# Performance work log

Hardware: AMD Instinct MI355X
Metric: run time of the kernel (lower is better)

Reference implementation:

```python
import jax, jax.numpy as jnp
import numpy as np

H = 1024        # hidden_dim
NH = 8          # num_heads
HD = H // NH    # head_dim
EPS = 1e-5


def setup_inputs() -> dict:
    key = jax.random.key(0)
    ks = jax.random.split(key, 16)
    s = 0.02
    d = {
        'x': jax.random.normal(ks[0], (2, 2048, H), dtype=jnp.float32),
        'ln1_g': jnp.ones((H,), jnp.float32), 'ln1_b': jnp.zeros((H,), jnp.float32),
        'ln2_g': jnp.ones((H,), jnp.float32), 'ln2_b': jnp.zeros((H,), jnp.float32),
        'Wq': jax.random.normal(ks[1], (H, H), jnp.float32) * s,
        'bq': jnp.zeros((H,), jnp.float32),
        'Wk': jax.random.normal(ks[2], (H, H), jnp.float32) * s,
        'bk': jnp.zeros((H,), jnp.float32),
        'Wv': jax.random.normal(ks[3], (H, H), jnp.float32) * s,
        'bv': jnp.zeros((H,), jnp.float32),
        'Wo': jax.random.normal(ks[4], (H, H), jnp.float32) * s,
        'bo': jnp.zeros((H,), jnp.float32),
        'W1': jax.random.normal(ks[5], (H, 4 * H), jnp.float32) * s,
        'b1': jnp.zeros((4 * H,), jnp.float32),
        'W2': jax.random.normal(ks[6], (4 * H, H), jnp.float32) * s,
        'b2': jnp.zeros((H,), jnp.float32),
    }
    return d


def _layernorm(x, g, b):
    mu = jnp.mean(x, axis=-1, keepdims=True)
    var = jnp.mean(jnp.square(x - mu), axis=-1, keepdims=True)
    return (x - mu) * jax.lax.rsqrt(var + EPS) * g + b


def _block(x, ln1_g, ln1_b, ln2_g, ln2_b, Wq, bq, Wk, bk, Wv, bv, Wo, bo, W1, b1, W2, b2):
    B, S, _ = x.shape
    h = _layernorm(x, ln1_g, ln1_b)
    q = (h @ Wq + bq).reshape(B, S, NH, HD).transpose(0, 2, 1, 3)  # [B,NH,S,HD]
    k = (h @ Wk + bk).reshape(B, S, NH, HD).transpose(0, 2, 1, 3)
    v = (h @ Wv + bv).reshape(B, S, NH, HD).transpose(0, 2, 1, 3)
    scores = jnp.einsum('bhqd,bhkd->bhqk', q, k) / np.sqrt(HD)
    causal = jnp.tril(jnp.ones((S, S), bool))
    scores = jnp.where(causal, scores, -jnp.inf)
    attn = jax.nn.softmax(scores, axis=-1)
    y = jnp.einsum('bhqk,bhkd->bhqd', attn, v).transpose(0, 2, 1, 3).reshape(B, S, H)
    x = x + y @ Wo + bo
    h2 = _layernorm(x, ln2_g, ln2_b)
    m = jax.nn.gelu(h2 @ W1 + b1, approximate=False) @ W2 + b2
    return x + m


def reference(x, ln1_g, ln1_b, ln2_g, ln2_b, Wq, bq, Wk, bk, Wv, bv, Wo, bo, W1, b1, W2, b2):
    return _block(x, ln1_g, ln1_b, ln2_g, ln2_b, Wq, bq, Wk, bk, Wv, bv, Wo, bo, W1, b1, W2, b2)
```

## Files before the change

kernel.cpp:

```cpp
#include <hip/hip_runtime.h>
#include <hip/hip_bf16.h>
#include <math.h>

using bf16 = __hip_bfloat16;
typedef __attribute__((ext_vector_type(8))) short short8v;
typedef __attribute__((ext_vector_type(4))) float f32x4;

#define DEV __device__ __forceinline__

DEV void load_lds16(const bf16* gsrc, bf16* ldst) {
  __builtin_amdgcn_global_load_lds((const __attribute__((address_space(1))) void*)gsrc,
                                   (__attribute__((address_space(3))) void*)ldst, 16, 0, 0);
}

DEV void swz8(int& bx, int& by, int gx, int gy) {
  const int n = gx * gy, c = n >> 3;
  int lin = bx + gx * by;
  lin = (lin & 7) * c + (lin >> 3);
  bx = lin % gx; by = lin / gx;
}

DEV unsigned pack2bf(float a, float b) {
  bf16 ba = __float2bfloat16(a), bb = __float2bfloat16(b);
  return (unsigned)*(unsigned short*)&ba | ((unsigned)*(unsigned short*)&bb << 16);
}

__global__ __launch_bounds__(256) void prep_kernel(
    const float* __restrict__ Wq, const float* __restrict__ Wk, const float* __restrict__ Wv,
    const float* __restrict__ Wo, const float* __restrict__ W1, const float* __restrict__ W2,
    bf16* __restrict__ WqT, bf16* __restrict__ WkT, bf16* __restrict__ WvT,
    bf16* __restrict__ WoT, bf16* __restrict__ W1T, bf16* __restrict__ W2T,
    const float* __restrict__ x, const float* __restrict__ ln1g, const float* __restrict__ ln1b,
    bf16* __restrict__ h) {
  __shared__ float tile[64][65];
  const int b = blockIdx.x;
  if (b >= 3072) {
    const int row = b - 3072, t = threadIdx.x;
    const float4 v = ((const float4*)(x + (size_t)row * 1024))[t];
    float s = v.x + v.y + v.z + v.w;
#pragma unroll
    for (int mm = 1; mm < 64; mm <<= 1) s += __shfl_xor(s, mm);
    __shared__ float r1[4], r2[4];
    if ((t & 63) == 0) r1[t >> 6] = s;
    __syncthreads();
    const float mean = (r1[0] + r1[1] + r1[2] + r1[3]) * (1.0f / 1024.0f);
    const float d0 = v.x - mean, d1 = v.y - mean, d2 = v.z - mean, d3 = v.w - mean;
    float s2 = d0 * d0 + d1 * d1 + d2 * d2 + d3 * d3;
#pragma unroll
    for (int mm = 1; mm < 64; mm <<= 1) s2 += __shfl_xor(s2, mm);
    if ((t & 63) == 0) r2[t >> 6] = s2;
    __syncthreads();
    const float var = (r2[0] + r2[1] + r2[2] + r2[3]) * (1.0f / 1024.0f);
    const float rinv = rsqrtf(var + 1e-5f);
    const int c = t * 4;
    bf16* o = h + (size_t)row * 1024 + c;
    o[0] = __float2bfloat16(d0 * rinv * ln1g[c + 0] + ln1b[c + 0]);
    o[1] = __float2bfloat16(d1 * rinv * ln1g[c + 1] + ln1b[c + 1]);
    o[2] = __float2bfloat16(d2 * rinv * ln1g[c + 2] + ln1b[c + 2]);
    o[3] = __float2bfloat16(d3 * rinv * ln1g[c + 3] + ln1b[c + 3]);
    return;
  }
  const float* W; bf16* WT; int K, N, n0, k0;
  if (b < 1024) {
    const int which = b >> 8, t = b & 255;
    W  = (which == 0) ? Wq  : (which == 1) ? Wk  : (which == 2) ? Wv  : Wo;
    WT = (which == 0) ? WqT : (which == 1) ? WkT : (which == 2) ? WvT : WoT;
    K = 1024; N = 1024; n0 = (t & 15) * 64; k0 = (t >> 4) * 64;
  } else if (b < 2048) {
    const int t = b - 1024;
    W = W1; WT = W1T; K = 1024; N = 4096; n0 = (t & 63) * 64; k0 = (t >> 6) * 64;
  } else {
    const int t = b - 2048;
    W = W2; WT = W2T; K = 4096; N = 1024; n0 = (t & 15) * 64; k0 = (t >> 4) * 64;
  }
  const int tx = threadIdx.x & 15, ty = threadIdx.x >> 4;
#pragma unroll
  for (int p = 0; p < 4; ++p) {
    int r = p * 16 + ty;
    float4 vv = *(const float4*)&W[(size_t)(k0 + r) * N + n0 + tx * 4];
    tile[r][tx * 4 + 0] = vv.x; tile[r][tx * 4 + 1] = vv.y;
    tile[r][tx * 4 + 2] = vv.z; tile[r][tx * 4 + 3] = vv.w;
  }
  __syncthreads();
#pragma unroll
  for (int p = 0; p < 4; ++p) {
    int n = p * 16 + ty;
    bf16* dst = WT + (size_t)(n0 + n) * K + k0 + tx * 4;
#pragma unroll
    for (int j = 0; j < 4; ++j) dst[j] = __float2bfloat16(tile[tx * 4 + j][n]);
  }
}

__global__ __launch_bounds__(256) void ln_kernel(const float* __restrict__ x,
                                                 const float* __restrict__ g,
                                                 const float* __restrict__ b,
                                                 bf16* __restrict__ out) {
  const int row = blockIdx.x, t = threadIdx.x;
  const float4 v = ((const float4*)(x + (size_t)row * 1024))[t];
  float s = v.x + v.y + v.z + v.w;
#pragma unroll
  for (int mm = 1; mm < 64; mm <<= 1) s += __shfl_xor(s, mm);
  __shared__ float r1[4], r2[4];
  if ((t & 63) == 0) r1[t >> 6] = s;
  __syncthreads();
  const float mean = (r1[0] + r1[1] + r1[2] + r1[3]) * (1.0f / 1024.0f);
  const float d0 = v.x - mean, d1 = v.y - mean, d2 = v.z - mean, d3 = v.w - mean;
  float s2 = d0 * d0 + d1 * d1 + d2 * d2 + d3 * d3;
#pragma unroll
  for (int mm = 1; mm < 64; mm <<= 1) s2 += __shfl_xor(s2, mm);
  if ((t & 63) == 0) r2[t >> 6] = s2;
  __syncthreads();
  const float var = (r2[0] + r2[1] + r2[2] + r2[3]) * (1.0f / 1024.0f);
  const float rinv = rsqrtf(var + 1e-5f);
  const int c = t * 4;
  bf16* o = out + (size_t)row * 1024 + c;
  o[0] = __float2bfloat16(d0 * rinv * g[c + 0] + b[c + 0]);
  o[1] = __float2bfloat16(d1 * rinv * g[c + 1] + b[c + 1]);
  o[2] = __float2bfloat16(d2 * rinv * g[c + 2] + b[c + 2]);
  o[3] = __float2bfloat16(d3 * rinv * g[c + 3] + b[c + 3]);
}

template <int EPI>
__global__ __launch_bounds__(512, 2) void gemm256(
    const bf16* __restrict__ A, const bf16* __restrict__ BT,
    const float* __restrict__ bias0, const float* __restrict__ bias1, const float* __restrict__ bias2,
    void* __restrict__ outp, int M, int N, int K) {
  __shared__ bf16 As[4][256 * 32];
  __shared__ bf16 Bs[4][256 * 32];
  const int tid = threadIdx.x;
  const int w = tid >> 6, l = tid & 63;
  const int wm = w >> 2, wn = w & 3;
  const int c = l & 15, h4 = l >> 4;
  int bx = blockIdx.x, by = blockIdx.y;
  swz8(bx, by, gridDim.x, gridDim.y);
  const int m0 = by * 256, n0 = bx * 256;

  const float* bias;
  int zz = 0;
  if (EPI == 0) {
    zz = n0 >> 10;
    bias = ((zz == 0) ? bias0 : (zz == 1) ? bias1 : bias2) - (zz << 10);
  } else {
    bias = bias0;
  }

  const int rl = l >> 2;
  const int ch = (l & 3) * 8;
  const int nkt = K >> 5;

  f32x4 acc[8][4] = {};

  auto STAGE_A = [&](int t, int b) {
    const bf16* src = A + (size_t)(m0 + rl) * K + t * 32 + ch;
    load_lds16(src + (size_t)((w * 2 + 0) * 16) * K, &As[b][(w * 2 + 0) * 512]);
    load_lds16(src + (size_t)((w * 2 + 1) * 16) * K, &As[b][(w * 2 + 1) * 512]);
  };
  auto STAGE_B = [&](int t, int b) {
    const bf16* src = BT + (size_t)(n0 + rl) * K + t * 32 + ch;
    load_lds16(src + (size_t)((w * 2 + 0) * 16) * K, &Bs[b][(w * 2 + 0) * 512]);
    load_lds16(src + (size_t)((w * 2 + 1) * 16) * K, &Bs[b][(w * 2 + 1) * 512]);
  };

  STAGE_A(0, 0); STAGE_B(0, 0);
  STAGE_A(1, 1); STAGE_B(1, 1);
  STAGE_A(2, 2); STAGE_B(2, 2);
  asm volatile("s_waitcnt vmcnt(8)" ::: "memory");
  __builtin_amdgcn_sched_barrier(0);
  __builtin_amdgcn_s_barrier();

  for (int t = 0; t < nkt; ++t) {
    const bf16* Ab = &As[t & 3][0];
    const bf16* Bb = &Bs[t & 3][0];
    short8v a[4], b[4];
#pragma unroll
    for (int i = 0; i < 4; ++i)
      a[i] = *(const short8v*)&Ab[(wm * 128 + i * 16 + c) * 32 + h4 * 8];
#pragma unroll
    for (int i = 0; i < 4; ++i)
      b[i] = *(const short8v*)&Bb[(wn * 64 + i * 16 + c) * 32 + h4 * 8];
    if (t + 3 < nkt) STAGE_A(t + 3, (t + 3) & 3);
    asm volatile("s_waitcnt lgkmcnt(0)" ::: "memory");
    __builtin_amdgcn_sched_barrier(0);
    __builtin_amdgcn_s_setprio(1);
#pragma unroll
    for (int mi = 0; mi < 4; ++mi)
#pragma unroll
      for (int ni = 0; ni < 4; ++ni)
        acc[mi][ni] = __builtin_amdgcn_mfma_f32_16x16x32_bf16(a[mi], b[ni], acc[mi][ni], 0, 0, 0);
    __builtin_amdgcn_s_setprio(0);
#pragma unroll
    for (int i = 0; i < 4; ++i)
      a[i] = *(const short8v*)&Ab[(wm * 128 + 64 + i * 16 + c) * 32 + h4 * 8];
    if (t + 3 < nkt) STAGE_B(t + 3, (t + 3) & 3);
    asm volatile("s_waitcnt lgkmcnt(0)" ::: "memory");
    __builtin_amdgcn_sched_barrier(0);
    __builtin_amdgcn_s_setprio(1);
#pragma unroll
    for (int mi = 0; mi < 4; ++mi)
#pragma unroll
      for (int ni = 0; ni < 4; ++ni)
        acc[4 + mi][ni] = __builtin_amdgcn_mfma_f32_16x16x32_bf16(a[mi], b[ni], acc[4 + mi][ni], 0, 0, 0);
    __builtin_amdgcn_s_setprio(0);
    if (t < nkt - 3)       asm volatile("s_waitcnt vmcnt(8)" ::: "memory");
    else if (t == nkt - 3) asm volatile("s_waitcnt vmcnt(4)" ::: "memory");
    else                   asm volatile("s_waitcnt vmcnt(0)" ::: "memory");
    __builtin_amdgcn_sched_barrier(0);
    __builtin_amdgcn_s_barrier();
  }

#pragma unroll
  for (int mi = 0; mi < 8; ++mi) {
#pragma unroll
    for (int ni = 0; ni < 4; ++ni) {
#pragma unroll
      for (int r = 0; r < 4; ++r) {
        const int m = m0 + wm * 128 + mi * 16 + h4 * 4 + r;
        const int n = n0 + wn * 64 + ni * 16 + c;
        const float vv = acc[mi][ni][r] + bias[n];
        if (EPI == 0) {
          const int bb = m >> 11, ss = m & 2047;
          const int n1 = n - (zz << 10);
          const int hh = n1 >> 7, dd = n1 & 127;
          ((bf16*)outp)[(size_t)zz * 4194304 + (((size_t)bb * 8 + hh) * 2048 + ss) * 128 + dd] =
              __float2bfloat16(vv);
        } else {
          const size_t idx = (size_t)m * N + n;
          const float u = 0.7978845608028654f * (vv + 0.044715f * vv * vv * vv);
          const float tt = __expf(2.0f * u);
          const float th = 1.0f - 2.0f / (tt + 1.0f);
          ((bf16*)outp)[idx] = __float2bfloat16(0.5f * vv * (1.0f + th));
        }
      }
    }
  }
}

template <int EPI, int MI>
__global__ __launch_bounds__(256) void gemm128(
    const bf16* __restrict__ A, const bf16* __restrict__ BT,
    const float* __restrict__ bias0, const float* __restrict__ bias1, const float* __restrict__ bias2,
    const float* __restrict__ res, void* __restrict__ outp,
    int M, int N, int K) {
  __shared__ bf16 As[2][MI * 1024];
  __shared__ bf16 Bs[2][128 * 32];
  const int tid = threadIdx.x;
  const int w = tid >> 6, l = tid & 63;
  const int wr = w >> 1, wc = w & 1;
  const int col = l & 15, hi = l >> 4;
  int bx = blockIdx.x, by = blockIdx.y;
  swz8(bx, by, gridDim.x, gridDim.y);
  const int m0 = by * (32 * MI), n0 = bx * 128;

  const float* bias = bias0;

  const int srow = l >> 2;
  const int scol = ((l & 3) ^ ((l >> 4) & 3)) * 8;
  const int rs = col * 4 + (hi ^ ((l >> 2) & 3));
  f32x4 acc[MI][4] = {};

  const int nk = K >> 5;
#pragma unroll
  for (int j = 0; j < MI / 2; ++j) {
    const int grp = w * (MI / 2) + j;
    load_lds16(A + (size_t)(m0 + grp * 16 + srow) * K + scol, &As[0][grp * 512]);
  }
#pragma unroll
  for (int j = 0; j < 2; ++j) {
    const int grp = w * 2 + j;
    load_lds16(BT + (size_t)(n0 + grp * 16 + srow) * K + scol, &Bs[0][grp * 512]);
  }
  __syncthreads();

  int cur = 0;
  for (int kt = 0; kt < nk; ++kt) {
    if (kt + 1 < nk) {
      const int k0n = (kt + 1) * 32;
#pragma unroll
      for (int j = 0; j < MI / 2; ++j) {
        const int grp = w * (MI / 2) + j;
        load_lds16(A + (size_t)(m0 + grp * 16 + srow) * K + k0n + scol, &As[cur ^ 1][grp * 512]);
      }
#pragma unroll
      for (int j = 0; j < 2; ++j) {
        const int grp = w * 2 + j;
        load_lds16(BT + (size_t)(n0 + grp * 16 + srow) * K + k0n + scol, &Bs[cur ^ 1][grp * 512]);
      }
    }
    __builtin_amdgcn_sched_barrier(0);

    short8v af[MI], bfr[4];
#pragma unroll
    for (int i = 0; i < MI; ++i)
      af[i] = *(const short8v*)&As[cur][(wr * MI + i) * 512 + rs * 8];
#pragma unroll
    for (int i = 0; i < 4; ++i)
      bfr[i] = *(const short8v*)&Bs[cur][(wc * 4 + i) * 512 + rs * 8];
#pragma unroll
    for (int mi = 0; mi < MI; ++mi)
#pragma unroll
      for (int ni = 0; ni < 4; ++ni)
        acc[mi][ni] = __builtin_amdgcn_mfma_f32_16x16x32_bf16(af[mi], bfr[ni], acc[mi][ni], 0, 0, 0);
    __syncthreads();
    cur ^= 1;
  }

#pragma unroll
  for (int mi = 0; mi < MI; ++mi) {
#pragma unroll
    for (int ni = 0; ni < 4; ++ni) {
#pragma unroll
      for (int r = 0; r < 4; ++r) {
        const int m = m0 + wr * (16 * MI) + mi * 16 + hi * 4 + r;
        const int n = n0 + wc * 64 + ni * 16 + col;
        const float vv = acc[mi][ni][r] + bias[n];
        const size_t idx = (size_t)m * N + n;
        ((float*)outp)[idx] = res[idx] + vv;
      }
    }
  }
}

__global__ __launch_bounds__(512, 1) void gemm_sk2(
    const bf16* __restrict__ A, const bf16* __restrict__ BT,
    const float* __restrict__ bias, const float* __restrict__ res, float* __restrict__ outp,
    int M, int N, int K) {
  __shared__ __align__(16) char lds_raw[131072];
  const int tid = threadIdx.x;
  const int w = tid >> 6, l = tid & 63;
  const int grp = w >> 2, wg = w & 3;
  const int wr = wg >> 1, wc = wg & 1;
  const int col = l & 15, hi = l >> 4;
  int bx = blockIdx.x, by = blockIdx.y;
  swz8(bx, by, gridDim.x, gridDim.y);
  const int m0 = by * 128, n0 = bx * 128;

  const int rl = l >> 2;
  const int ch = (l & 3) * 8;
  f32x4 acc[4][4] = {};

  const int KH = K >> 1;
  const int kbase = grp * KH;
  const int nkt = KH >> 5;

  auto ABUF = [&](int b) { return (bf16*)(lds_raw + grp * 65536 + b * 16384); };
  auto BBUF = [&](int b) { return (bf16*)(lds_raw + grp * 65536 + b * 16384 + 8192); };

  auto STAGE = [&](int t, int b) {
    const bf16* srcA = A + (size_t)(m0 + rl) * K + kbase + t * 32 + ch;
    const bf16* srcB = BT + (size_t)(n0 + rl) * K + kbase + t * 32 + ch;
    bf16* Ab = ABUF(b); bf16* Bb = BBUF(b);
    load_lds16(srcA + (size_t)((wg * 2 + 0) * 16) * K, Ab + (wg * 2 + 0) * 512);
    load_lds16(srcA + (size_t)((wg * 2 + 1) * 16) * K, Ab + (wg * 2 + 1) * 512);
    load_lds16(srcB + (size_t)((wg * 2 + 0) * 16) * K, Bb + (wg * 2 + 0) * 512);
    load_lds16(srcB + (size_t)((wg * 2 + 1) * 16) * K, Bb + (wg * 2 + 1) * 512);
  };

  STAGE(0, 0); STAGE(1, 1); STAGE(2, 2);
  asm volatile("s_waitcnt vmcnt(8)" ::: "memory");
  __builtin_amdgcn_sched_barrier(0);
  __builtin_amdgcn_s_barrier();

  for (int t = 0; t < nkt; ++t) {
    const bf16* Ab = ABUF(t & 3);
    const bf16* Bb = BBUF(t & 3);
    short8v af[4], bf_[4];
#pragma unroll
    for (int i = 0; i < 4; ++i) {
      af[i]  = *(const short8v*)&Ab[(wr * 64 + i * 16 + col) * 32 + hi * 8];
      bf_[i] = *(const short8v*)&Bb[(wc * 64 + i * 16 + col) * 32 + hi * 8];
    }
    if (t + 3 < nkt) STAGE(t + 3, (t + 3) & 3);
    asm volatile("s_waitcnt lgkmcnt(0)" ::: "memory");
    __builtin_amdgcn_sched_barrier(0);
    __builtin_amdgcn_s_setprio(1);
#pragma unroll
    for (int mi = 0; mi < 4; ++mi)
#pragma unroll
      for (int ni = 0; ni < 4; ++ni)
        acc[mi][ni] = __builtin_amdgcn_mfma_f32_16x16x32_bf16(af[mi], bf_[ni], acc[mi][ni], 0, 0, 0);
    __builtin_amdgcn_s_setprio(0);
    if (t < nkt - 3)       asm volatile("s_waitcnt vmcnt(8)" ::: "memory");
    else if (t == nkt - 3) asm volatile("s_waitcnt vmcnt(4)" ::: "memory");
    else                   asm volatile("s_waitcnt vmcnt(0)" ::: "memory");
    __builtin_amdgcn_sched_barrier(0);
    __builtin_amdgcn_s_barrier();
  }

  float* dump = (float*)lds_raw;
  if (grp == 1) {
#pragma unroll
    for (int mi = 0; mi < 4; ++mi)
#pragma unroll
      for (int ni = 0; ni < 4; ++ni)
#pragma unroll
        for (int r = 0; r < 4; ++r)
          dump[(wr * 64 + mi * 16 + hi * 4 + r) * 130 + wc * 64 + ni * 16 + col] = acc[mi][ni][r];
  }
  __syncthreads();
  if (grp == 0) {
#pragma unroll
    for (int mi = 0; mi < 4; ++mi) {
#pragma unroll
      for (int ni = 0; ni < 4; ++ni) {
#pragma unroll
        for (int r = 0; r < 4; ++r) {
          const int lrow = wr * 64 + mi * 16 + hi * 4 + r;
          const int lcol = wc * 64 + ni * 16 + col;
          const int m = m0 + lrow, n = n0 + lcol;
          const size_t idx = (size_t)m * N + n;
          outp[idx] = res[idx] + acc[mi][ni][r] + dump[lrow * 130 + lcol] + bias[n];
        }
      }
    }
  }
}

__global__ __launch_bounds__(512) void attn_kernel(const bf16* __restrict__ q,
                                                   const bf16* __restrict__ k,
                                                   const bf16* __restrict__ v,
                                                   bf16* __restrict__ y) {
  __shared__ __align__(16) char lds_raw[157696];
  int p = blockIdx.x, bh = blockIdx.y;
  swz8(p, bh, 16, 16);
  const int tid = threadIdx.x;
  const int w = tid >> 6, l = tid & 63;
  const int grp = w >> 2, wg = w & 3;
  const int col = l & 15, hi = l >> 4;

  const bf16* kbase = k + (size_t)bh * 2048 * 128;
  const bf16* vbase = v + (size_t)bh * 2048 * 128;
  const int bb = bh >> 3, hh = bh & 7;

  bf16* Psw = (bf16*)(lds_raw + 139264 + (size_t)w * 2304);

  const int klr = (l >> 4);
  const int kblk0 = l & 15;
  const int vr = (l & 31) * 2;
  const int vcb = (wg * 2 + (l >> 5)) * 16;

  const float scale = 0.08838834764831845f;

  for (int half = 0; half < 2; ++half) {
    const int qt = half ? p : (31 - p);
    const int q0 = qt * 64;
    const int T = qt + 1;
    const int n0 = (T + 1) >> 1;
    const int myn = grp ? (T >> 1) : n0;
    const int tb = grp ? n0 : 0;

    short8v qf[4];
    const bf16* qp = q + ((size_t)bh * 2048 + q0 + wg * 16 + col) * 128;
#pragma unroll
    for (int c = 0; c < 4; ++c) qf[c] = *(const short8v*)(qp + c * 32 + hi * 8);

    f32x4 o[8] = {};
    float mx = -1e30f, sm = 0.f;

    if (myn > 0) {
      bf16* Ks0 = (bf16*)(lds_raw + (size_t)(grp * 2 + 0) * 16384);
      bf16* Vt0 = (bf16*)(lds_raw + 65536 + (size_t)(grp * 2 + 0) * 18432);
#pragma unroll
      for (int j = 0; j < 4; ++j) {
        const int lr = j * 4 + klr;
        const int blk = kblk0 ^ (lr & 7);
        load_lds16(kbase + (size_t)(tb * 64 + wg * 16 + lr) * 128 + blk * 8,
                   Ks0 + wg * 2048 + j * 512);
      }
      const bf16* vsrc = vbase + (size_t)(tb * 64 + vr) * 128 + vcb;
      short8v v00 = *(const short8v*)vsrc;
      short8v v01 = *(const short8v*)(vsrc + 8);
      short8v v10 = *(const short8v*)(vsrc + 128);
      short8v v11 = *(const short8v*)(vsrc + 136);
#pragma unroll
      for (int i = 0; i < 8; ++i) {
        *(unsigned int*)&Vt0[(vcb + i) * 72 + vr] =
            ((unsigned int)(unsigned short)v00[i]) | (((unsigned int)(unsigned short)v10[i]) << 16);
        *(unsigned int*)&Vt0[(vcb + 8 + i) * 72 + vr] =
            ((unsigned int)(unsigned short)v01[i]) | (((unsigned int)(unsigned short)v11[i]) << 16);
      }
    }
    __syncthreads();

    for (int it = 0; it < n0; ++it) {
      const int cur = it & 1;
      const bool active = it < myn;
      const bool havenext = (it + 1) < myn;
      bf16* KsCur = (bf16*)(lds_raw + (size_t)(grp * 2 + cur) * 16384);
      bf16* KsNxt = (bf16*)(lds_raw + (size_t)(grp * 2 + (cur ^ 1)) * 16384);
      bf16* VtCur = (bf16*)(lds_raw + 65536 + (size_t)(grp * 2 + cur) * 18432);
      bf16* VtNxt = (bf16*)(lds_raw + 65536 + (size_t)(grp * 2 + (cur ^ 1)) * 18432);

      short8v v00, v01, v10, v11;
      if (havenext) {
        const int nt = tb + it + 1;
#pragma unroll
        for (int j = 0; j < 4; ++j) {
          const int lr = j * 4 + klr;
          const int blk = kblk0 ^ (lr & 7);
          load_lds16(kbase + (size_t)(nt * 64 + wg * 16 + lr) * 128 + blk * 8,
                     KsNxt + wg * 2048 + j * 512);
        }
        const bf16* vsrc = vbase + (size_t)(nt * 64 + vr) * 128 + vcb;
        v00 = *(const short8v*)vsrc;
        v01 = *(const short8v*)(vsrc + 8);
        v10 = *(const short8v*)(vsrc + 128);
        v11 = *(const short8v*)(vsrc + 136);
      }

      if (active) {
        const int ktile = tb + it;
        f32x4 s[4] = {};
        __builtin_amdgcn_s_setprio(1);
#pragma unroll
        for (int c4 = 0; c4 < 4; ++c4) {
#pragma unroll
          for (int kg = 0; kg < 4; ++kg) {
            const int kr = kg * 16 + col;
            short8v kf = *(const short8v*)&KsCur[kr * 128 + ((c4 * 32 + hi * 8) ^ ((col & 7) << 3))];
            s[kg] = __builtin_amdgcn_mfma_f32_16x16x32_bf16(kf, qf[c4], s[kg], 0, 0, 0);
          }
        }
        __builtin_amdgcn_s_setprio(0);

        const bool diag = (ktile == qt);
        const int qloc = wg * 16 + col;
#pragma unroll
        for (int kg = 0; kg < 4; ++kg) {
#pragma unroll
          for (int r = 0; r < 4; ++r) {
            float a = s[kg][r] * scale;
            if (diag && (kg * 16 + hi * 4 + r > qloc)) a = -1e30f;
            s[kg][r] = a;
          }
        }
        f32x4 m4;
#pragma unroll
        for (int r = 0; r < 4; ++r)
          m4[r] = fmaxf(fmaxf(s[0][r], s[1][r]), fmaxf(s[2][r], s[3][r]));
        float t = fmaxf(fmaxf(m4[0], m4[1]), fmaxf(m4[2], m4[3]));
        t = fmaxf(t, __shfl_xor(t, 16));
        t = fmaxf(t, __shfl_xor(t, 32));
        const float mn = fmaxf(mx, t);
        const float aa = __expf(mx - mn);
        float ps = 0.f;
        unsigned pk0[4], pk1[4];
#pragma unroll
        for (int kg = 0; kg < 4; ++kg) {
          const float p0 = __expf(s[kg][0] - mn);
          const float p1 = __expf(s[kg][1] - mn);
          const float p2 = __expf(s[kg][2] - mn);
          const float p3 = __expf(s[kg][3] - mn);
          ps += (p0 + p1) + (p2 + p3);
          pk0[kg] = pack2bf(p0, p1);
          pk1[kg] = pack2bf(p2, p3);
        }
        ps += __shfl_xor(ps, 16);
        ps += __shfl_xor(ps, 32);
        sm = sm * aa + ps;
        mx = mn;
#pragma unroll
        for (int kg = 0; kg < 4; ++kg) {
          *(unsigned*)&Psw[col * 72 + kg * 16 + hi * 4]     = pk0[kg];
          *(unsigned*)&Psw[col * 72 + kg * 16 + hi * 4 + 2] = pk1[kg];
        }
#pragma unroll
        for (int db = 0; db < 8; ++db) {
          o[db][0] *= aa; o[db][1] *= aa; o[db][2] *= aa; o[db][3] *= aa;
        }
      }

      if (havenext) {
#pragma unroll
        for (int i = 0; i < 8; ++i) {
          *(unsigned int*)&VtNxt[(vcb + i) * 72 + vr] =
              ((unsigned int)(unsigned short)v00[i]) | (((unsigned int)(unsigned short)v10[i]) << 16);
          *(unsigned int*)&VtNxt[(vcb + 8 + i) * 72 + vr] =
              ((unsigned int)(unsigned short)v01[i]) | (((unsigned int)(unsigned short)v11[i]) << 16);
        }
      }

      if (active) {
        asm volatile("s_waitcnt lgkmcnt(0)" ::: "memory");
        __builtin_amdgcn_s_setprio(1);
#pragma unroll
        for (int ks = 0; ks < 2; ++ks) {
          short8v pf = *(const short8v*)&Psw[col * 72 + ks * 32 + hi * 8];
#pragma unroll
          for (int db = 0; db < 8; ++db) {
            short8v vf = *(const short8v*)&VtCur[(db * 16 + col) * 72 + ks * 32 + hi * 8];
            o[db] = __builtin_amdgcn_mfma_f32_16x16x32_bf16(vf, pf, o[db], 0, 0, 0);
          }
        }
        __builtin_amdgcn_s_setprio(0);
      }
      __syncthreads();
    }

    if (grp == 1) {
      float* Mo = (float*)(lds_raw + (size_t)wg * 8448);
      float* Ml = (float*)(lds_raw + 33792 + (size_t)wg * 128);
#pragma unroll
      for (int db = 0; db < 8; ++db)
        *(f32x4*)&Mo[col * 132 + db * 16 + hi * 4] = o[db];
      if (hi == 0) { Ml[col * 2] = mx; Ml[col * 2 + 1] = sm; }
    }
    __syncthreads();
    if (grp == 0) {
      const float* Mo = (const float*)(lds_raw + (size_t)wg * 8448);
      const float* Ml = (const float*)(lds_raw + 33792 + (size_t)wg * 128);
      const float m1 = Ml[col * 2], l1 = Ml[col * 2 + 1];
      const float M = fmaxf(mx, m1);
      const float a0 = __expf(mx - M);
      const float a1 = __expf(m1 - M);
      const float inv = 1.0f / (sm * a0 + l1 * a1);
      const int qg = q0 + wg * 16 + col;
      bf16* yrow = y + ((size_t)bb * 2048 + qg) * 1024 + hh * 128;
#pragma unroll
      for (int db = 0; db < 8; ++db) {
        f32x4 rd = *(const f32x4*)&Mo[col * 132 + db * 16 + hi * 4];
        const unsigned w0 = pack2bf((o[db][0] * a0 + rd[0] * a1) * inv,
                                    (o[db][1] * a0 + rd[1] * a1) * inv);
        const unsigned w1 = pack2bf((o[db][2] * a0 + rd[2] * a1) * inv,
                                    (o[db][3] * a0 + rd[3] * a1) * inv);
        uint2 pk; pk.x = w0; pk.y = w1;
        *(uint2*)(yrow + db * 16 + hi * 4) = pk;
      }
    }
    __syncthreads();
  }
}

extern "C" void kernel_launch(void* const* d_in, const int* in_sizes, int n_in,
                              void* d_out, int out_size, void* d_ws, size_t ws_size,
                              hipStream_t stream) {
  const float* x    = (const float*)d_in[0];
  const float* ln1g = (const float*)d_in[1];
  const float* ln1b = (const float*)d_in[2];
  const float* ln2g = (const float*)d_in[3];
  const float* ln2b = (const float*)d_in[4];
  const float* Wq   = (const float*)d_in[5];
  const float* bq   = (const float*)d_in[6];
  const float* Wk   = (const float*)d_in[7];
  const float* bk   = (const float*)d_in[8];
  const float* Wv   = (const float*)d_in[9];
  const float* bv   = (const float*)d_in[10];
  const float* Wo   = (const float*)d_in[11];
  const float* bo   = (const float*)d_in[12];
  const float* W1   = (const float*)d_in[13];
  const float* b1   = (const float*)d_in[14];
  const float* W2   = (const float*)d_in[15];
  const float* b2   = (const float*)d_in[16];
  float* out = (float*)d_out;
  char* ws = (char*)d_ws;
  const size_t MB = 1024 * 1024;

  bf16* WqT = (bf16*)(ws + 0 * MB);
  bf16* WkT = (bf16*)(ws + 2 * MB);
  bf16* WvT = (bf16*)(ws + 4 * MB);
  bf16* WoT = (bf16*)(ws + 6 * MB);
  bf16* W1T = (bf16*)(ws + 8 * MB);
  bf16* W2T = (bf16*)(ws + 16 * MB);
  bf16* h   = (bf16*)(ws + 24 * MB);
  bf16* qb  = (bf16*)(ws + 32 * MB);
  bf16* kb  = (bf16*)(ws + 40 * MB);
  bf16* vb  = (bf16*)(ws + 48 * MB);
  bf16* y   = (bf16*)(ws + 56 * MB);
  bf16* g   = (bf16*)(ws + 32 * MB);
  float* x1 = (float*)(ws + 64 * MB);
  bf16* h2  = h;

  prep_kernel<<<7168, 256, 0, stream>>>(Wq, Wk, Wv, Wo, W1, W2, WqT, WkT, WvT, WoT, W1T, W2T,
                                        x, ln1g, ln1b, h);

  gemm256<0><<<dim3(12, 16), 512, 0, stream>>>(h, WqT, bq, bk, bv, qb, 4096, 3072, 1024);

  attn_kernel<<<dim3(16, 16), 512, 0, stream>>>(qb, kb, vb, y);

  gemm128<1, 2><<<dim3(8, 64), 256, 0, stream>>>(y, WoT, bo, nullptr, nullptr, x, x1,
                                                 4096, 1024, 1024);

  ln_kernel<<<4096, 256, 0, stream>>>(x1, ln2g, ln2b, h2);

  gemm256<2><<<dim3(16, 16), 512, 0, stream>>>(h2, W1T, b1, nullptr, nullptr, g,
                                               4096, 4096, 1024);

  gemm_sk2<<<dim3(8, 32), 512, 0, stream>>>(g, W2T, b2, x1, out, 4096, 1024, 4096);
}
```

Baseline: 220.9 us.

## Switch attention to 32x32 MFMA with key-split waves, lazy rescale, prescaled Q

```diff
diff --git a/kernel.cpp b/kernel.cpp
--- a/kernel.cpp
+++ b/kernel.cpp
@@ -5,6 +5,7 @@
 using bf16 = __hip_bfloat16;
 typedef __attribute__((ext_vector_type(8))) short short8v;
 typedef __attribute__((ext_vector_type(4))) float f32x4;
+typedef __attribute__((ext_vector_type(16))) float f32x16;
 
 #define DEV __device__ __forceinline__
 
@@ -216,8 +217,9 @@
       for (int r = 0; r < 4; ++r) {
         const int m = m0 + wm * 128 + mi * 16 + h4 * 4 + r;
         const int n = n0 + wn * 64 + ni * 16 + c;
-        const float vv = acc[mi][ni][r] + bias[n];
+        float vv = acc[mi][ni][r] + bias[n];
         if (EPI == 0) {
+          if (zz == 0) vv *= 0.08838834764831845f;
           const int bb = m >> 11, ss = m & 2047;
           const int n1 = n - (zz << 10);
           const int hh = n1 >> 7, dd = n1 & 127;
@@ -419,26 +421,28 @@
                                                    const bf16* __restrict__ k,
                                                    const bf16* __restrict__ v,
                                                    bf16* __restrict__ y) {
-  __shared__ __align__(16) char lds_raw[157696];
+  __shared__ __align__(16) char lds_raw[159744];
   int p = blockIdx.x, bh = blockIdx.y;
   swz8(p, bh, 16, 16);
   const int tid = threadIdx.x;
   const int w = tid >> 6, l = tid & 63;
-  const int grp = w >> 2, wg = w & 3;
-  const int col = l & 15, hi = l >> 4;
+  const int grp = w >> 2;
+  const int wg  = w & 3;
+  const int qs  = (w >> 1) & 1;
+  const int ks  = w & 1;
+  const int lq  = l & 31;
+  const int lh  = l >> 5;
 
   const bf16* kbase = k + (size_t)bh * 2048 * 128;
   const bf16* vbase = v + (size_t)bh * 2048 * 128;
   const int bb = bh >> 3, hh = bh & 7;
 
-  bf16* Psw = (bf16*)(lds_raw + 139264 + (size_t)w * 2304);
+  bf16* Psw = (bf16*)(lds_raw + 139264 + (size_t)w * 2560);
 
   const int klr = (l >> 4);
   const int kblk0 = l & 15;
   const int vr = (l & 31) * 2;
   const int vcb = (wg * 2 + (l >> 5)) * 16;
-
-  const float scale = 0.08838834764831845f;
 
   for (int half = 0; half < 2; ++half) {
     const int qt = half ? p : (31 - p);
@@ -448,13 +452,13 @@
     const int myn = grp ? (T >> 1) : n0;
     const int tb = grp ? n0 : 0;
 
-    short8v qf[4];
-    const bf16* qp = q + ((size_t)bh * 2048 + q0 + wg * 16 + col) * 128;
-#pragma unroll
-    for (int c = 0; c < 4; ++c) qf[c] = *(const short8v*)(qp + c * 32 + hi * 8);
-
-    f32x4 o[8] = {};
-    float mx = -1e30f, sm = 0.f;
+    short8v qf[8];
+    const bf16* qp = q + ((size_t)bh * 2048 + q0 + qs * 32 + lq) * 128 + lh * 8;
+#pragma unroll
+    for (int c = 0; c < 8; ++c) qf[c] = *(const short8v*)(qp + c * 16);
+
+    f32x16 o[4] = {};
+    float mx = -1e20f, sm = 0.f;
 
     if (myn > 0) {
       bf16* Ks0 = (bf16*)(lds_raw + (size_t)(grp * 2 + 0) * 16384);
@@ -509,63 +513,60 @@
 
       if (active) {
         const int ktile = tb + it;
-        f32x4 s[4] = {};
+        f32x16 s = {};
+        const int kr = ks * 32 + lq;
+        const int swz = kr & 7;
         __builtin_amdgcn_s_setprio(1);
 #pragma unroll
-        for (int c4 = 0; c4 < 4; ++c4) {
-#pragma unroll
-          for (int kg = 0; kg < 4; ++kg) {
-            const int kr = kg * 16 + col;
-            short8v kf = *(const short8v*)&KsCur[kr * 128 + ((c4 * 32 + hi * 8) ^ ((col & 7) << 3))];
-            s[kg] = __builtin_amdgcn_mfma_f32_16x16x32_bf16(kf, qf[c4], s[kg], 0, 0, 0);
+        for (int c = 0; c < 8; ++c) {
+          const int gneed = 2 * c + lh;
+          short8v kf = *(const short8v*)&KsCur[kr * 128 + ((gneed ^ swz) << 3)];
+          s = __builtin_amdgcn_mfma_f32_32x32x16_bf16(kf, qf[c], s, 0, 0, 0);
+        }
+        __builtin_amdgcn_s_setprio(0);
+
+        if (ktile == qt) {
+          const int qloc = qs * 32 + lq;
+#pragma unroll
+          for (int reg = 0; reg < 16; ++reg) {
+            const int kloc = ks * 32 + (reg & 3) + 8 * (reg >> 2) + 4 * lh;
+            if (kloc > qloc) s[reg] = -1e30f;
           }
         }
-        __builtin_amdgcn_s_setprio(0);
-
-        const bool diag = (ktile == qt);
-        const int qloc = wg * 16 + col;
-#pragma unroll
-        for (int kg = 0; kg < 4; ++kg) {
-#pragma unroll
-          for (int r = 0; r < 4; ++r) {
-            float a = s[kg][r] * scale;
-            if (diag && (kg * 16 + hi * 4 + r > qloc)) a = -1e30f;
-            s[kg][r] = a;
-          }
-        }
-        f32x4 m4;
-#pragma unroll
-        for (int r = 0; r < 4; ++r)
-          m4[r] = fmaxf(fmaxf(s[0][r], s[1][r]), fmaxf(s[2][r], s[3][r]));
-        float t = fmaxf(fmaxf(m4[0], m4[1]), fmaxf(m4[2], m4[3]));
-        t = fmaxf(t, __shfl_xor(t, 16));
+        float t0 = fmaxf(fmaxf(s[0], s[1]), fmaxf(s[2], s[3]));
+        float t1 = fmaxf(fmaxf(s[4], s[5]), fmaxf(s[6], s[7]));
+        float t2 = fmaxf(fmaxf(s[8], s[9]), fmaxf(s[10], s[11]));
+        float t3 = fmaxf(fmaxf(s[12], s[13]), fmaxf(s[14], s[15]));
+        float t = fmaxf(fmaxf(t0, t1), fmaxf(t2, t3));
         t = fmaxf(t, __shfl_xor(t, 32));
-        const float mn = fmaxf(mx, t);
-        const float aa = __expf(mx - mn);
+        float mn;
+        if (__all(t <= mx + 8.0f)) {
+          mn = mx;
+        } else {
+          mn = fmaxf(mx, t);
+          const float aa = __expf(mx - mn);
+          sm *= aa;
+#pragma unroll
+          for (int db = 0; db < 4; ++db) o[db] *= aa;
+          mx = mn;
+        }
         float ps = 0.f;
-        unsigned pk0[4], pk1[4];
-#pragma unroll
-        for (int kg = 0; kg < 4; ++kg) {
-          const float p0 = __expf(s[kg][0] - mn);
-          const float p1 = __expf(s[kg][1] - mn);
-          const float p2 = __expf(s[kg][2] - mn);
-          const float p3 = __expf(s[kg][3] - mn);
+        unsigned u[8];
+#pragma unroll
+        for (int rq = 0; rq < 4; ++rq) {
+          const float p0 = __expf(s[rq * 4 + 0] - mn);
+          const float p1 = __expf(s[rq * 4 + 1] - mn);
+          const float p2 = __expf(s[rq * 4 + 2] - mn);
+          const float p3 = __expf(s[rq * 4 + 3] - mn);
           ps += (p0 + p1) + (p2 + p3);
-          pk0[kg] = pack2bf(p0, p1);
-          pk1[kg] = pack2bf(p2, p3);
-        }
-        ps += __shfl_xor(ps, 16);
-        ps += __shfl_xor(ps, 32);
-        sm = sm * aa + ps;
-        mx = mn;
-#pragma unroll
-        for (int kg = 0; kg < 4; ++kg) {
-          *(unsigned*)&Psw[col * 72 + kg * 16 + hi * 4]     = pk0[kg];
-          *(unsigned*)&Psw[col * 72 + kg * 16 + hi * 4 + 2] = pk1[kg];
-        }
-#pragma unroll
-        for (int db = 0; db < 8; ++db) {
-          o[db][0] *= aa; o[db][1] *= aa; o[db][2] *= aa; o[db][3] *= aa;
+          u[rq * 2 + 0] = pack2bf(p0, p1);
+          u[rq * 2 + 1] = pack2bf(p2, p3);
+        }
+        sm += ps;
+#pragma unroll
+        for (int rq = 0; rq < 4; ++rq) {
+          uint2 pk; pk.x = u[rq * 2]; pk.y = u[rq * 2 + 1];
+          *(uint2*)&Psw[lq * 40 + rq * 8 + lh * 4] = pk;
         }
       }
 
@@ -583,12 +584,12 @@
         asm volatile("s_waitcnt lgkmcnt(0)" ::: "memory");
         __builtin_amdgcn_s_setprio(1);
 #pragma unroll
-        for (int ks = 0; ks < 2; ++ks) {
-          short8v pf = *(const short8v*)&Psw[col * 72 + ks * 32 + hi * 8];
-#pragma unroll
-          for (int db = 0; db < 8; ++db) {
-            short8v vf = *(const short8v*)&VtCur[(db * 16 + col) * 72 + ks * 32 + hi * 8];
-            o[db] = __builtin_amdgcn_mfma_f32_16x16x32_bf16(vf, pf, o[db], 0, 0, 0);
+        for (int kc = 0; kc < 2; ++kc) {
+          short8v pf = *(const short8v*)&Psw[lq * 40 + kc * 16 + lh * 8];
+#pragma unroll
+          for (int db = 0; db < 4; ++db) {
+            short8v vf = *(const short8v*)&VtCur[(db * 32 + lq) * 72 + ks * 32 + kc * 16 + lh * 8];
+            o[db] = __builtin_amdgcn_mfma_f32_32x32x16_bf16(vf, pf, o[db], 0, 0, 0);
           }
         }
         __builtin_amdgcn_s_setprio(0);
@@ -596,34 +597,55 @@
       __syncthreads();
     }
 
-    if (grp == 1) {
-      float* Mo = (float*)(lds_raw + (size_t)wg * 8448);
-      float* Ml = (float*)(lds_raw + 33792 + (size_t)wg * 128);
-#pragma unroll
-      for (int db = 0; db < 8; ++db)
-        *(f32x4*)&Mo[col * 132 + db * 16 + hi * 4] = o[db];
-      if (hi == 0) { Ml[col * 2] = mx; Ml[col * 2 + 1] = sm; }
+    sm += __shfl_xor(sm, 32);
+
+    float* smmx = (float*)(lds_raw + 139264);
+    if (l < 32) { smmx[w * 64 + l] = sm; smmx[w * 64 + 32 + l] = mx; }
+    const bool merger = (grp == 0 && ks == 0);
+    if (!merger) {
+      const int slot = qs * 3 + (grp * 2 + ks - 1);
+      float* dst = (float*)(lds_raw + slot * 17408);
+#pragma unroll
+      for (int db = 0; db < 4; ++db) {
+#pragma unroll
+        for (int rq = 0; rq < 4; ++rq) {
+          f32x4 vv;
+          vv[0] = o[db][rq * 4 + 0]; vv[1] = o[db][rq * 4 + 1];
+          vv[2] = o[db][rq * 4 + 2]; vv[3] = o[db][rq * 4 + 3];
+          *(f32x4*)&dst[lq * 132 + db * 32 + rq * 8 + lh * 4] = vv;
+        }
+      }
     }
     __syncthreads();
-    if (grp == 0) {
-      const float* Mo = (const float*)(lds_raw + (size_t)wg * 8448);
-      const float* Ml = (const float*)(lds_raw + 33792 + (size_t)wg * 128);
-      const float m1 = Ml[col * 2], l1 = Ml[col * 2 + 1];
-      const float M = fmaxf(mx, m1);
-      const float a0 = __expf(mx - M);
-      const float a1 = __expf(m1 - M);
-      const float inv = 1.0f / (sm * a0 + l1 * a1);
-      const int qg = q0 + wg * 16 + col;
+    if (merger) {
+      const int w01 = w + 1, w10 = 4 + qs * 2, w11 = 5 + qs * 2;
+      const float sm01 = smmx[w01 * 64 + lq], mx01 = smmx[w01 * 64 + 32 + lq];
+      const float sm10 = smmx[w10 * 64 + lq], mx10 = smmx[w10 * 64 + 32 + lq];
+      const float sm11 = smmx[w11 * 64 + lq], mx11 = smmx[w11 * 64 + 32 + lq];
+      const float M = fmaxf(fmaxf(mx, mx01), fmaxf(mx10, mx11));
+      const float a00 = __expf(mx - M), a01 = __expf(mx01 - M);
+      const float a10 = __expf(mx10 - M), a11 = __expf(mx11 - M);
+      const float inv = 1.0f / (sm * a00 + sm01 * a01 + sm10 * a10 + sm11 * a11);
+      const float* d01 = (const float*)(lds_raw + (qs * 3 + 0) * 17408);
+      const float* d10 = (const float*)(lds_raw + (qs * 3 + 1) * 17408);
+      const float* d11 = (const float*)(lds_raw + (qs * 3 + 2) * 17408);
+      const int qg = q0 + qs * 32 + lq;
       bf16* yrow = y + ((size_t)bb * 2048 + qg) * 1024 + hh * 128;
 #pragma unroll
-      for (int db = 0; db < 8; ++db) {
-        f32x4 rd = *(const f32x4*)&Mo[col * 132 + db * 16 + hi * 4];
-        const unsigned w0 = pack2bf((o[db][0] * a0 + rd[0] * a1) * inv,
-                                    (o[db][1] * a0 + rd[1] * a1) * inv);
-        const unsigned w1 = pack2bf((o[db][2] * a0 + rd[2] * a1) * inv,
-                                    (o[db][3] * a0 + rd[3] * a1) * inv);
-        uint2 pk; pk.x = w0; pk.y = w1;
-        *(uint2*)(yrow + db * 16 + hi * 4) = pk;
+      for (int db = 0; db < 4; ++db) {
+#pragma unroll
+        for (int rq = 0; rq < 4; ++rq) {
+          const int off = lq * 132 + db * 32 + rq * 8 + lh * 4;
+          const f32x4 v01 = *(const f32x4*)&d01[off];
+          const f32x4 v10 = *(const f32x4*)&d10[off];
+          const f32x4 v11 = *(const f32x4*)&d11[off];
+          const float r0 = (o[db][rq * 4 + 0] * a00 + v01[0] * a01 + v10[0] * a10 + v11[0] * a11) * inv;
+          const float r1 = (o[db][rq * 4 + 1] * a00 + v01[1] * a01 + v10[1] * a10 + v11[1] * a11) * inv;
+          const float r2 = (o[db][rq * 4 + 2] * a00 + v01[2] * a01 + v10[2] * a10 + v11[2] * a11) * inv;
+          const float r3 = (o[db][rq * 4 + 3] * a00 + v01[3] * a01 + v10[3] * a10 + v11[3] * a11) * inv;
+          uint2 pk; pk.x = pack2bf(r0, r1); pk.y = pack2bf(r2, r3);
+          *(uint2*)(yrow + db * 32 + rq * 8 + lh * 4) = pk;
+        }
       }
     }
     __syncthreads();
```

Measured after the change: 227.1 us. 2.8% more time.
